# Performance work log

Measured on AMD Instinct MI355X. Metric: run time of the kernel, lower is better.

The kernel has to match this reference:

```python
import jax, jax.numpy as jnp
import numpy as np

N_NODES = 50000
N_EDGES = 800000
IN_CH = 64
OC = 16  # out_channels


def setup_inputs() -> dict:
    key = jax.random.key(0)
    ks = jax.random.split(key, 16)
    x = jax.random.normal(ks[0], (N_NODES, IN_CH), dtype=jnp.float32)
    edge_index = jax.random.randint(ks[1], (2, N_EDGES), 0, N_NODES, dtype=jnp.int64)

    def lin(k, fan_in, fan_out):
        s = 1.0 / np.sqrt(fan_in)
        return jax.random.uniform(k, (fan_in, fan_out), jnp.float32, -s, s)

    d1, d2 = 16 * OC, 8 * OC  # 256, 128
    return {
        "x": x,
        "W1_rel": lin(ks[2], IN_CH, d1), "b1": jnp.zeros((d1,), jnp.float32), "W1_root": lin(ks[3], IN_CH, d1),
        "W2_rel": lin(ks[4], d1, d2), "b2": jnp.zeros((d2,), jnp.float32), "W2_root": lin(ks[5], d1, d2),
        "Wmu_rel": lin(ks[6], d2, OC), "bmu": jnp.zeros((OC,), jnp.float32), "Wmu_root": lin(ks[7], d2, OC),
        "Wls_rel": lin(ks[8], d2, OC), "bls": jnp.zeros((OC,), jnp.float32), "Wls_root": lin(ks[9], d2, OC),
        "edge_index": edge_index,
    }


def _graph_conv(x, src, dst, deg_inv, W_rel, b, W_root):
    # PyG GraphConv(aggr='mean'): out = lin_rel(mean_{j in N(i)} x_j) + lin_root(x_i)
    msg_sum = jax.ops.segment_sum(x[src], dst, num_segments=x.shape[0])  # [N, d]
    agg = msg_sum * deg_inv[:, None]
    return agg @ W_rel + b + x @ W_root


def reference(x, W1_rel, b1, W1_root, W2_rel, b2, W2_root,
              Wmu_rel, bmu, Wmu_root, Wls_rel, bls, Wls_root, edge_index):
    src, dst = edge_index[0], edge_index[1]
    deg = jax.ops.segment_sum(jnp.ones_like(dst, dtype=x.dtype), dst, num_segments=x.shape[0])
    deg_inv = jnp.where(deg > 0, 1.0 / jnp.maximum(deg, 1.0), 0.0)

    h = jax.nn.relu(_graph_conv(x, src, dst, deg_inv, W1_rel, b1, W1_root))
    h = jax.nn.relu(_graph_conv(h, src, dst, deg_inv, W2_rel, b2, W2_root))
    mu = _graph_conv(h, src, dst, deg_inv, Wmu_rel, bmu, Wmu_root)
    logstd = _graph_conv(h, src, dst, deg_inv, Wls_rel, bls, Wls_root)
    return (mu, logstd)
```

## Files before the change

### kernel.cpp

```cpp
#include <hip/hip_runtime.h>
#include <hip/hip_fp8.h>

#define N_NODES 50000
#define N_EDGES 800000
#define NBUCK 196
#define PBLK 391
#define CAP 5120

typedef unsigned short ushort_t;
typedef unsigned char uchar_t;
typedef short short8 __attribute__((ext_vector_type(8)));
typedef short short4v __attribute__((ext_vector_type(4)));
typedef float floatx4 __attribute__((ext_vector_type(4)));
typedef float floatx2 __attribute__((ext_vector_type(2)));

__device__ __forceinline__ float bf2f(ushort_t u) {
    unsigned v = ((unsigned)u) << 16;
    return __builtin_bit_cast(float, v);
}
__device__ __forceinline__ ushort_t f2bf(float f) {
    unsigned u = __builtin_bit_cast(unsigned, f);
    unsigned r = (u + 0x7FFFu + ((u >> 16) & 1u)) >> 16;
    return (ushort_t)r;
}
__device__ __forceinline__ uchar_t f2fp8(float f) {
    return (uchar_t)(__builtin_amdgcn_cvt_pk_fp8_f32(f, f, 0, false) & 0xFF);
}
__device__ __forceinline__ float4 ld4(const float* p) { return *(const float4*)p; }

__device__ __forceinline__ void lite_barrier() {
    asm volatile("s_waitcnt lgkmcnt(0)" ::: "memory");
    __builtin_amdgcn_s_barrier();
}

__device__ __forceinline__ void acc16(float* a, uint4 v) {
    unsigned ws[4] = {v.x, v.y, v.z, v.w};
    #pragma unroll
    for (int wi = 0; wi < 4; ++wi) {
        floatx2 lo = __builtin_amdgcn_cvt_pk_f32_fp8(ws[wi], false);
        floatx2 hi = __builtin_amdgcn_cvt_pk_f32_fp8(ws[wi], true);
        a[wi * 4 + 0] += lo.x; a[wi * 4 + 1] += lo.y;
        a[wi * 4 + 2] += hi.x; a[wi * 4 + 3] += hi.y;
    }
}
__device__ __forceinline__ void acc8(float* a, uint2 v) {
    floatx2 p0 = __builtin_amdgcn_cvt_pk_f32_fp8(v.x, false);
    floatx2 p1 = __builtin_amdgcn_cvt_pk_f32_fp8(v.x, true);
    floatx2 p2 = __builtin_amdgcn_cvt_pk_f32_fp8(v.y, false);
    floatx2 p3 = __builtin_amdgcn_cvt_pk_f32_fp8(v.y, true);
    a[0] += p0.x; a[1] += p0.y; a[2] += p1.x; a[3] += p1.y;
    a[4] += p2.x; a[5] += p2.y; a[6] += p3.x; a[7] += p3.y;
}

__global__ __launch_bounds__(256) void prep_kernel(
    const float* __restrict__ x,
    const float* __restrict__ W1_rel, const float* __restrict__ W1_root,
    const float* __restrict__ W2_rel, const float* __restrict__ W2_root,
    const float* __restrict__ Wmu_rel, const float* __restrict__ Wls_rel,
    const float* __restrict__ Wmu_root, const float* __restrict__ Wls_root,
    ushort_t* __restrict__ xb, uchar_t* __restrict__ xq,
    ushort_t* __restrict__ B1t, ushort_t* __restrict__ B2t, ushort_t* __restrict__ B3t,
    int* __restrict__ bcursor) {
    int idx = blockIdx.x * blockDim.x + threadIdx.x;
    if (idx < 400000) {
        int n = idx >> 3, c = (idx & 7) * 8;
        float4 v0 = ld4(x + (size_t)n * 64 + c);
        float4 v1 = ld4(x + (size_t)n * 64 + c + 4);
        float vv[8] = {v0.x, v0.y, v0.z, v0.w, v1.x, v1.y, v1.z, v1.w};
        short8 o;
        #pragma unroll
        for (int i = 0; i < 8; ++i) o[i] = f2bf(vv[i]);
        int q0 = __builtin_amdgcn_cvt_pk_fp8_f32(vv[0], vv[1], 0, false);
        q0 = __builtin_amdgcn_cvt_pk_fp8_f32(vv[2], vv[3], q0, true);
        int q1 = __builtin_amdgcn_cvt_pk_fp8_f32(vv[4], vv[5], 0, false);
        q1 = __builtin_amdgcn_cvt_pk_fp8_f32(vv[6], vv[7], q1, true);
        *(short8*)(xb + (size_t)n * 64 + c) = o;
        uint2 q = {(unsigned)q0, (unsigned)q1};
        *(uint2*)(xq + (size_t)n * 64 + c) = q;
    } else if (idx < 506496) {
        int j = idx - 400000;
        if (j < 32768) {
            int n = j >> 7, k = j & 127;
            float v = (k < 64) ? W1_rel[k * 256 + n] : W1_root[(k - 64) * 256 + n];
            B1t[j] = f2bf(v);
        } else if (j < 98304) {
            int jj = j - 32768;
            int n = jj >> 8, k = jj & 255;
            float v = (n < 128) ? W2_rel[k * 128 + n] : W2_root[k * 128 + (n - 128)];
            B2t[jj] = f2bf(v);
        } else {
            int jj = j - 98304;
            int n = jj >> 7, k = jj & 127;
            const float* W = (n < 16) ? Wmu_rel : (n < 32) ? Wls_rel : (n < 48) ? Wmu_root : Wls_root;
            B3t[jj] = f2bf(W[k * 16 + (n & 15)]);
        }
    } else if (idx < 506496 + NBUCK) {
        int b = idx - 506496;
        bcursor[b] = b * CAP;
    }
}

__global__ __launch_bounds__(512) void partition_kernel(
    const int* __restrict__ src, const int* __restrict__ dst,
    int* __restrict__ bcursor, unsigned* __restrict__ pairbuf) {
    __shared__ int h[NBUCK];
    __shared__ int cur[NBUCK];
    const int tid = threadIdx.x;
    for (int i = tid; i < NBUCK; i += 512) h[i] = 0;
    __syncthreads();
    const int base = blockIdx.x * 2048;
    int d[4];
    #pragma unroll
    for (int j = 0; j < 4; ++j) {
        int e = base + j * 512 + tid;
        if (e < N_EDGES) { d[j] = dst[e]; atomicAdd(&h[d[j] >> 8], 1); }
        else d[j] = -1;
    }
    __syncthreads();
    for (int i = tid; i < NBUCK; i += 512) {
        int c = h[i];
        cur[i] = c ? atomicAdd(&bcursor[i], c) : 0;
    }
    __syncthreads();
    #pragma unroll
    for (int j = 0; j < 4; ++j) {
        int e = base + j * 512 + tid;
        if (e < N_EDGES) {
            int dd = d[j];
            int slot = atomicAdd(&cur[dd >> 8], 1);
            pairbuf[slot] = (unsigned)src[e] | ((unsigned)(dd & 255) << 16);
        }
    }
}

__global__ __launch_bounds__(1024) void fill_bucket_kernel(
    const unsigned* __restrict__ pairbuf, const int* __restrict__ bcursor,
    int* __restrict__ row_beg, int* __restrict__ row_end,
    float* __restrict__ dinv, ushort_t* __restrict__ eidx) {
    __shared__ int h[256];
    __shared__ int sm[256];
    __shared__ int cur[256];
    const int b = blockIdx.x, tid = threadIdx.x;
    const int beg = b * CAP, end = bcursor[b];
    if (tid < 256) h[tid] = 0;
    __syncthreads();
    for (int i = beg + tid; i < end; i += 1024)
        atomicAdd(&h[pairbuf[i] >> 16], 1);
    __syncthreads();
    if (tid < 256) sm[tid] = h[tid];
    __syncthreads();
    #pragma unroll
    for (int off = 1; off < 256; off <<= 1) {
        int t = 0;
        if (tid < 256 && tid >= off) t = sm[tid - off];
        __syncthreads();
        if (tid < 256) sm[tid] += t;
        __syncthreads();
    }
    if (tid < 256) {
        int c = h[tid];
        int exc = beg + sm[tid] - c;
        int node = b * 256 + tid;
        if (node < N_NODES) {
            row_beg[node] = exc;
            row_end[node] = exc + c;
            dinv[node] = c > 0 ? 1.0f / (float)c : 0.0f;
        }
        cur[tid] = exc;
    }
    __syncthreads();
    for (int i = beg + tid; i < end; i += 1024) {
        unsigned v = pairbuf[i];
        int slot = atomicAdd(&cur[v >> 16], 1);
        eidx[slot] = (ushort_t)(v & 0xFFFFu);
    }
}

__global__ __launch_bounds__(256, 3) void g1gemm12(
    const ushort_t* __restrict__ xb, const uchar_t* __restrict__ xq,
    const int* __restrict__ row_beg, const int* __restrict__ row_end,
    const ushort_t* __restrict__ eidx, const float* __restrict__ dinv,
    const ushort_t* __restrict__ B1t, const float* __restrict__ b1,
    const ushort_t* __restrict__ B2t,
    uchar_t* __restrict__ t2, ushort_t* __restrict__ r2) {
    constexpr int K1 = 128, K2 = 256;
    constexpr int AKP = 72;
    constexpr int HKP = 264;
    constexpr int BKP = 136;
    __shared__ ushort_t Bs[64 * BKP];
    __shared__ ushort_t Hs[64 * HKP];
    ushort_t* As = Bs;
    const int tid = threadIdx.x;
    const int rowbase = blockIdx.x * 64;

    {
        const int nl = tid >> 2, lane = tid & 3;
        const int node = rowbase + nl;
        int beg = 0, end = 0;
        float d = 0.0f;
        if (node < N_NODES) { beg = row_beg[node]; end = row_end[node]; d = dinv[node]; }
        float a0[16] = {}, a1[16] = {};
        int j = beg;
        for (; j + 3 < end; j += 4) {
            uint4 v0 = *(const uint4*)(xq + (size_t)eidx[j] * 64 + lane * 16);
            uint4 v1 = *(const uint4*)(xq + (size_t)eidx[j + 1] * 64 + lane * 16);
            uint4 v2 = *(const uint4*)(xq + (size_t)eidx[j + 2] * 64 + lane * 16);
            uint4 v3 = *(const uint4*)(xq + (size_t)eidx[j + 3] * 64 + lane * 16);
            acc16(a0, v0); acc16(a1, v1); acc16(a0, v2); acc16(a1, v3);
        }
        for (; j < end; ++j) {
            uint4 v0 = *(const uint4*)(xq + (size_t)eidx[j] * 64 + lane * 16);
            acc16(a0, v0);
        }
        short8 o0, o1;
        #pragma unroll
        for (int i = 0; i < 8; ++i) {
            o0[i] = f2bf((a0[i] + a1[i]) * d);
            o1[i] = f2bf((a0[8 + i] + a1[8 + i]) * d);
        }
        *(short8*)(As + nl * AKP + lane * 16) = o0;
        *(short8*)(As + nl * AKP + lane * 16 + 8) = o1;
    }
    __syncthreads();

    const int w = tid >> 6, lane64 = tid & 63;
    const int ln = lane64 & 15, quad = lane64 >> 4;
    const int rwl = w * 16 + ln;
    int r = rowbase + rwl;
    if (r > N_NODES - 1) r = N_NODES - 1;

    float bias[4][4];
    #pragma unroll
    for (int ny = 0; ny < 4; ++ny)
        #pragma unroll
        for (int f = 0; f < 4; ++f)
            bias[ny][f] = b1[ny * 64 + f * 16 + ln];

    short8 a[4];
    a[0] = *(const short8*)(As + rwl * AKP + quad * 8);
    a[1] = *(const short8*)(As + rwl * AKP + 32 + quad * 8);
    a[2] = *(const short8*)(xb + (size_t)r * 64 + quad * 8);
    a[3] = *(const short8*)(xb + (size_t)r * 64 + 32 + quad * 8);
    {
        short8 pb[4];
        #pragma unroll
        for (int i = 0; i < 4; ++i) {
            int idx = tid + i * 256, row = idx >> 4, off = (idx & 15) * 8;
            pb[i] = *(const short8*)(B1t + (size_t)row * K1 + off);
        }
        for (int ny = 0; ny < 4; ++ny) {
            lite_barrier();
            #pragma unroll
            for (int i = 0; i < 4; ++i) {
                int idx = tid + i * 256, row = idx >> 4, off = (idx & 15) * 8;
                *(short8*)(Bs + row * BKP + off) = pb[i];
            }
            if (ny < 3) {
                #pragma unroll
                for (int i = 0; i < 4; ++i) {
                    int idx = tid + i * 256, row = idx >> 4, off = (idx & 15) * 8;
                    pb[i] = *(const short8*)(B1t + (size_t)((ny + 1) * 64 + row) * K1 + off);
                }
            }
            lite_barrier();
            floatx4 acc[4] = {};
            #pragma unroll
            for (int f = 0; f < 4; ++f) {
                const ushort_t* bp = Bs + (f * 16 + ln) * BKP + quad * 8;
                #pragma unroll
                for (int s = 0; s < 4; ++s) {
                    short8 b = *(const short8*)(bp + s * 32);
                    acc[f] = __builtin_amdgcn_mfma_f32_16x16x32_bf16(a[s], b, acc[f], 0, 0, 0);
                }
            }
            #pragma unroll
            for (int f = 0; f < 4; ++f) {
                int n = ny * 64 + f * 16 + ln;
                #pragma unroll
                for (int g = 0; g < 4; ++g) {
                    int rr = w * 16 + quad * 4 + g;
                    Hs[rr * HKP + n] = f2bf(fmaxf(acc[f][g] + bias[ny][f], 0.0f));
                }
            }
        }
    }
    __syncthreads();

    short8 a2[8];
    #pragma unroll
    for (int s = 0; s < 8; ++s)
        a2[s] = *(const short8*)(Hs + rwl * HKP + s * 32 + quad * 8);
    ushort_t* Or16 = Hs;
    uchar_t*  Ot8  = (uchar_t*)(Hs + 8704);
    {
        short8 pb[4];
        #pragma unroll
        for (int i = 0; i < 4; ++i) {
            int idx = tid + i * 256, row = idx >> 4, off = (idx & 15) * 8;
            pb[i] = *(const short8*)(B2t + (size_t)row * K2 + off);
        }
        for (int ny = 0; ny < 4; ++ny) {
            floatx4 acc[4] = {};
            #pragma unroll
            for (int kh = 0; kh < 2; ++kh) {
                lite_barrier();
                #pragma unroll
                for (int i = 0; i < 4; ++i) {
                    int idx = tid + i * 256, row = idx >> 4, off = (idx & 15) * 8;
                    *(short8*)(Bs + row * BKP + off) = pb[i];
                }
                int st = ny * 2 + kh;
                if (st < 7) {
                    int nyn = (st + 1) >> 1, khn = (st + 1) & 1;
                    #pragma unroll
                    for (int i = 0; i < 4; ++i) {
                        int idx = tid + i * 256, row = idx >> 4, off = (idx & 15) * 8;
                        pb[i] = *(const short8*)(B2t + (size_t)(nyn * 64 + row) * K2 + khn * 128 + off);
                    }
                }
                lite_barrier();
                #pragma unroll
                for (int f = 0; f < 4; ++f) {
                    const ushort_t* bp = Bs + (f * 16 + ln) * BKP + quad * 8;
                    #pragma unroll
                    for (int s = 0; s < 4; ++s) {
                        short8 b = *(const short8*)(bp + s * 32);
                        acc[f] = __builtin_amdgcn_mfma_f32_16x16x32_bf16(a2[kh * 4 + s], b, acc[f], 0, 0, 0);
                    }
                }
            }
            #pragma unroll
            for (int f = 0; f < 4; ++f) {
                int n = ny * 64 + f * 16 + ln;
                #pragma unroll
                for (int g = 0; g < 4; ++g) {
                    int rr = w * 16 + quad * 4 + g;
                    float v = acc[f][g];
                    if (n < 128) Ot8[rr * 144 + n] = f2fp8(v);
                    else Or16[rr * 136 + (n - 128)] = f2bf(v);
                }
            }
        }
    }
    __syncthreads();

    {
        const int row = tid >> 2, seg = tid & 3;
        const int gr = rowbase + row;
        if (gr < N_NODES) {
            const uint4* ps = (const uint4*)(Ot8 + row * 144 + seg * 32);
            uint4* pd = (uint4*)(t2 + (size_t)gr * 128 + seg * 32);
            pd[0] = ps[0]; pd[1] = ps[1];
            const uint4* qs = (const uint4*)(Or16 + row * 136 + seg * 32);
            uint4* qd = (uint4*)(r2 + (size_t)gr * 128 + seg * 32);
            qd[0] = qs[0]; qd[1] = qs[1]; qd[2] = qs[2]; qd[3] = qs[3];
        }
    }
}

__global__ __launch_bounds__(256) void g2g3_kernel(
    const uchar_t* __restrict__ t2, const ushort_t* __restrict__ r2,
    const int* __restrict__ row_beg, const int* __restrict__ row_end,
    const ushort_t* __restrict__ eidx, const float* __restrict__ dinv,
    const float* __restrict__ b2, const ushort_t* __restrict__ B3t,
    ushort_t* __restrict__ tml, float* __restrict__ rml) {
    constexpr int KP = 136;
    __shared__ ushort_t As[16 * KP];
    const int tid = threadIdx.x;
    const int nb = blockIdx.x * 16;
    {
        const int nl = tid >> 4, lane = tid & 15;
        const int node = nb + nl;
        const int beg = row_beg[node], end = row_end[node];
        float a0[8] = {}, a1[8] = {}, a2[8] = {}, a3[8] = {};
        int j = beg;
        for (; j + 3 < end; j += 4) {
            uint2 v0 = *(const uint2*)(t2 + (size_t)eidx[j] * 128 + lane * 8);
            uint2 v1 = *(const uint2*)(t2 + (size_t)eidx[j + 1] * 128 + lane * 8);
            uint2 v2 = *(const uint2*)(t2 + (size_t)eidx[j + 2] * 128 + lane * 8);
            uint2 v3 = *(const uint2*)(t2 + (size_t)eidx[j + 3] * 128 + lane * 8);
            acc8(a0, v0); acc8(a1, v1); acc8(a2, v2); acc8(a3, v3);
        }
        for (; j < end; ++j) {
            uint2 v0 = *(const uint2*)(t2 + (size_t)eidx[j] * 128 + lane * 8);
            acc8(a0, v0);
        }
        float d = dinv[node];
        short8 rv = *(const short8*)(r2 + (size_t)node * 128 + lane * 8);
        float4 ba = ld4(b2 + lane * 8), bb = ld4(b2 + lane * 8 + 4);
        float bc[8] = {ba.x, ba.y, ba.z, ba.w, bb.x, bb.y, bb.z, bb.w};
        short8 o;
        #pragma unroll
        for (int i = 0; i < 8; ++i)
            o[i] = f2bf(fmaxf(((a0[i] + a1[i]) + (a2[i] + a3[i])) * d + bf2f((ushort_t)rv[i]) + bc[i], 0.0f));
        *(short8*)(As + nl * KP + lane * 8) = o;
    }
    __syncthreads();
    const int w = tid >> 6, lane64 = tid & 63;
    const int ln = lane64 & 15, quad = lane64 >> 4;
    short8 a[4];
    #pragma unroll
    for (int s = 0; s < 4; ++s)
        a[s] = *(const short8*)(As + ln * KP + s * 32 + quad * 8);
    floatx4 acc = {};
    const ushort_t* bp = B3t + (size_t)(w * 16 + ln) * 128 + quad * 8;
    #pragma unroll
    for (int s = 0; s < 4; ++s) {
        short8 b = *(const short8*)(bp + s * 32);
        acc = __builtin_amdgcn_mfma_f32_16x16x32_bf16(a[s], b, acc, 0, 0, 0);
    }
    const int r0 = nb + quad * 4;
    const int ncol = w * 16 + ln;
    #pragma unroll
    for (int g = 0; g < 4; ++g) {
        int rr = r0 + g;
        float v = acc[g];
        if (ncol < 32) tml[(size_t)rr * 32 + ncol] = f2bf(v);
        else rml[(size_t)rr * 32 + (ncol - 32)] = v;
    }
}

__global__ __launch_bounds__(256) void gather3_kernel(
    const ushort_t* __restrict__ tml, const float* __restrict__ rml,
    const int* __restrict__ row_beg, const int* __restrict__ row_end,
    const ushort_t* __restrict__ eidx, const float* __restrict__ dinv,
    const float* __restrict__ bmu, const float* __restrict__ bls,
    float* __restrict__ out) {
    const int lane = threadIdx.x & 7;
    const int nl = threadIdx.x >> 3;
    const int n = blockIdx.x * 32 + nl;
    if (n >= N_NODES) return;
    const int beg = row_beg[n], end = row_end[n];
    float a0[4] = {}, a1[4] = {}, a2[4] = {}, a3[4] = {};
    int j = beg;
    for (; j + 3 < end; j += 4) {
        short4v v0 = *(const short4v*)(tml + (size_t)eidx[j] * 32 + lane * 4);
        short4v v1 = *(const short4v*)(tml + (size_t)eidx[j + 1] * 32 + lane * 4);
        short4v v2 = *(const short4v*)(tml + (size_t)eidx[j + 2] * 32 + lane * 4);
        short4v v3 = *(const short4v*)(tml + (size_t)eidx[j + 3] * 32 + lane * 4);
        #pragma unroll
        for (int i = 0; i < 4; ++i) {
            a0[i] += bf2f((ushort_t)v0[i]); a1[i] += bf2f((ushort_t)v1[i]);
            a2[i] += bf2f((ushort_t)v2[i]); a3[i] += bf2f((ushort_t)v3[i]);
        }
    }
    for (; j < end; ++j) {
        short4v v0 = *(const short4v*)(tml + (size_t)eidx[j] * 32 + lane * 4);
        #pragma unroll
        for (int i = 0; i < 4; ++i) a0[i] += bf2f((ushort_t)v0[i]);
    }
    float d = dinv[n];
    const float* bias = (lane < 4) ? (bmu + lane * 4) : (bls + (lane - 4) * 4);
    float4 ra = ld4(rml + (size_t)n * 32 + lane * 4);
    float4 ba = ld4(bias);
    float rr[4] = {ra.x, ra.y, ra.z, ra.w};
    float bc[4] = {ba.x, ba.y, ba.z, ba.w};
    float res[4];
    #pragma unroll
    for (int i = 0; i < 4; ++i) res[i] = ((a0[i] + a1[i]) + (a2[i] + a3[i])) * d + rr[i] + bc[i];
    float* base = (lane < 4) ? (out + (size_t)n * 16 + lane * 4)
                             : (out + 800000u + (size_t)n * 16 + (lane - 4) * 4);
    *(float4*)(base) = make_float4(res[0], res[1], res[2], res[3]);
}

extern "C" void kernel_launch(void* const* d_in, const int* in_sizes, int n_in,
                              void* d_out, int out_size, void* d_ws, size_t ws_size,
                              hipStream_t stream) {
    const float* x       = (const float*)d_in[0];
    const float* W1_rel  = (const float*)d_in[1];
    const float* b1      = (const float*)d_in[2];
    const float* W1_root = (const float*)d_in[3];
    const float* W2_rel  = (const float*)d_in[4];
    const float* b2      = (const float*)d_in[5];
    const float* W2_root = (const float*)d_in[6];
    const float* Wmu_rel = (const float*)d_in[7];
    const float* bmu     = (const float*)d_in[8];
    const float* Wmu_root= (const float*)d_in[9];
    const float* Wls_rel = (const float*)d_in[10];
    const float* bls     = (const float*)d_in[11];
    const float* Wls_root= (const float*)d_in[12];
    const int*   ei      = (const int*)d_in[13];
    const int* src = ei;
    const int* dst = ei + N_EDGES;

    int*      bcursor = (int*)d_ws;
    int*      row_beg = bcursor + 256;
    int*      row_end = row_beg + 50048;
    unsigned* pairbuf = (unsigned*)(row_end + 50048);
    ushort_t* eidx    = (ushort_t*)(pairbuf + 1003520);
    float*    dinv    = (float*)(eidx + 1003520);
    ushort_t* xb   = (ushort_t*)(dinv + 50000);
    uchar_t*  xq   = (uchar_t*)(xb + 3200000);
    uchar_t*  t2   = xq + 3200000;
    ushort_t* r2   = (ushort_t*)(t2 + 6400000);
    ushort_t* tml  = r2 + 6400000;
    ushort_t* B1t  = tml + 1600000;
    ushort_t* B2t  = B1t + 32768;
    ushort_t* B3t  = B2t + 65536;
    float* rml     = (float*)(B3t + 8192);
    float* out     = (float*)d_out;

    prep_kernel<<<1980, 256, 0, stream>>>(x, W1_rel, W1_root, W2_rel, W2_root,
                                          Wmu_rel, Wls_rel, Wmu_root, Wls_root,
                                          xb, xq, B1t, B2t, B3t, bcursor);
    partition_kernel<<<PBLK, 512, 0, stream>>>(src, dst, bcursor, pairbuf);
    fill_bucket_kernel<<<NBUCK, 1024, 0, stream>>>(pairbuf, bcursor, row_beg, row_end, dinv, eidx);

    g1gemm12<<<782, 256, 0, stream>>>(xb, xq, row_beg, row_end, eidx, dinv,
                                      B1t, b1, B2t, t2, r2);

    g2g3_kernel<<<3125, 256, 0, stream>>>(t2, r2, row_beg, row_end, eidx, dinv, b2, B3t, tml, rml);

    gather3_kernel<<<1563, 256, 0, stream>>>(tml, rml, row_beg, row_end, eidx, dinv, bmu, bls, out);
}
```

Measured before the change: 194.6 us.

## Spill layer-1 hidden tile to global scratch to shrink shared memory footprint

Removes the 64x264 bf16 shared buffer for the layer-1 hidden activations and writes each 64-column chunk to a global scratch buffer h1g through the small Bs staging area. The second GEMM then loads its A operand straight from global memory. The aim is to cut LDS per block, from roughly 51KB to roughly 17KB, so more blocks fit per CU. The cost is extra global write and read traffic, since the reads should mostly hit in L2, plus more barriers. The launch-bounds occupancy hint is also dropped.

Result: no change. 192.7 us (-1.0%).

```diff
diff --git a/kernel.cpp b/kernel.cpp
--- a/kernel.cpp
+++ b/kernel.cpp
@@ -176,19 +176,17 @@
     }
 }
 
-__global__ __launch_bounds__(256, 3) void g1gemm12(
+__global__ __launch_bounds__(256) void g1gemm12(
     const ushort_t* __restrict__ xb, const uchar_t* __restrict__ xq,
     const int* __restrict__ row_beg, const int* __restrict__ row_end,
     const ushort_t* __restrict__ eidx, const float* __restrict__ dinv,
     const ushort_t* __restrict__ B1t, const float* __restrict__ b1,
-    const ushort_t* __restrict__ B2t,
+    const ushort_t* __restrict__ B2t, ushort_t* __restrict__ h1g,
     uchar_t* __restrict__ t2, ushort_t* __restrict__ r2) {
     constexpr int K1 = 128, K2 = 256;
     constexpr int AKP = 72;
-    constexpr int HKP = 264;
     constexpr int BKP = 136;
     __shared__ ushort_t Bs[64 * BKP];
-    __shared__ ushort_t Hs[64 * HKP];
     ushort_t* As = Bs;
     const int tid = threadIdx.x;
     const int rowbase = blockIdx.x * 64;
@@ -241,119 +239,136 @@
     a[1] = *(const short8*)(As + rwl * AKP + 32 + quad * 8);
     a[2] = *(const short8*)(xb + (size_t)r * 64 + quad * 8);
     a[3] = *(const short8*)(xb + (size_t)r * 64 + 32 + quad * 8);
-    {
-        short8 pb[4];
+    short8 pb[4];
+    #pragma unroll
+    for (int i = 0; i < 4; ++i) {
+        int idx = tid + i * 256, row = idx >> 4, off = (idx & 15) * 8;
+        pb[i] = *(const short8*)(B1t + (size_t)row * K1 + off);
+    }
+    for (int ny = 0; ny < 4; ++ny) {
+        lite_barrier();
         #pragma unroll
         for (int i = 0; i < 4; ++i) {
             int idx = tid + i * 256, row = idx >> 4, off = (idx & 15) * 8;
-            pb[i] = *(const short8*)(B1t + (size_t)row * K1 + off);
-        }
-        for (int ny = 0; ny < 4; ++ny) {
+            *(short8*)(Bs + row * BKP + off) = pb[i];
+        }
+        if (ny < 3) {
+            #pragma unroll
+            for (int i = 0; i < 4; ++i) {
+                int idx = tid + i * 256, row = idx >> 4, off = (idx & 15) * 8;
+                pb[i] = *(const short8*)(B1t + (size_t)((ny + 1) * 64 + row) * K1 + off);
+            }
+        } else {
+            #pragma unroll
+            for (int i = 0; i < 4; ++i) {
+                int idx = tid + i * 256, row = idx >> 4, off = (idx & 15) * 8;
+                pb[i] = *(const short8*)(B2t + (size_t)row * K2 + off);
+            }
+        }
+        lite_barrier();
+        floatx4 acc[4] = {};
+        #pragma unroll
+        for (int f = 0; f < 4; ++f) {
+            const ushort_t* bp = Bs + (f * 16 + ln) * BKP + quad * 8;
+            #pragma unroll
+            for (int s = 0; s < 4; ++s) {
+                short8 b = *(const short8*)(bp + s * 32);
+                acc[f] = __builtin_amdgcn_mfma_f32_16x16x32_bf16(a[s], b, acc[f], 0, 0, 0);
+            }
+        }
+        lite_barrier();
+        #pragma unroll
+        for (int f = 0; f < 4; ++f) {
+            int nl0 = f * 16 + ln;
+            #pragma unroll
+            for (int g = 0; g < 4; ++g) {
+                int rr = w * 16 + quad * 4 + g;
+                Bs[rr * AKP + nl0] = f2bf(fmaxf(acc[f][g] + bias[ny][f], 0.0f));
+            }
+        }
+        lite_barrier();
+        {
+            int row2 = tid >> 2, seg = tid & 3;
+            int gr = rowbase + row2;
+            if (gr < N_NODES) {
+                const uint4* s4 = (const uint4*)(Bs + row2 * AKP + seg * 16);
+                uint4* d4 = (uint4*)(h1g + (size_t)gr * 256 + ny * 64 + seg * 16);
+                d4[0] = s4[0]; d4[1] = s4[1];
+            }
+        }
+    }
+    __syncthreads();
+
+    short8 a2[8];
+    #pragma unroll
+    for (int s = 0; s < 8; ++s)
+        a2[s] = *(const short8*)(h1g + (size_t)r * 256 + s * 32 + quad * 8);
+    for (int ny = 0; ny < 4; ++ny) {
+        floatx4 acc[4] = {};
+        #pragma unroll
+        for (int kh = 0; kh < 2; ++kh) {
             lite_barrier();
             #pragma unroll
             for (int i = 0; i < 4; ++i) {
                 int idx = tid + i * 256, row = idx >> 4, off = (idx & 15) * 8;
                 *(short8*)(Bs + row * BKP + off) = pb[i];
             }
-            if (ny < 3) {
+            int st = ny * 2 + kh;
+            if (st < 7) {
+                int nyn = (st + 1) >> 1, khn = (st + 1) & 1;
                 #pragma unroll
                 for (int i = 0; i < 4; ++i) {
                     int idx = tid + i * 256, row = idx >> 4, off = (idx & 15) * 8;
-                    pb[i] = *(const short8*)(B1t + (size_t)((ny + 1) * 64 + row) * K1 + off);
+                    pb[i] = *(const short8*)(B2t + (size_t)(nyn * 64 + row) * K2 + khn * 128 + off);
                 }
             }
             lite_barrier();
-            floatx4 acc[4] = {};
             #pragma unroll
             for (int f = 0; f < 4; ++f) {
                 const ushort_t* bp = Bs + (f * 16 + ln) * BKP + quad * 8;
                 #pragma unroll
                 for (int s = 0; s < 4; ++s) {
                     short8 b = *(const short8*)(bp + s * 32);
-                    acc[f] = __builtin_amdgcn_mfma_f32_16x16x32_bf16(a[s], b, acc[f], 0, 0, 0);
+                    acc[f] = __builtin_amdgcn_mfma_f32_16x16x32_bf16(a2[kh * 4 + s], b, acc[f], 0, 0, 0);
                 }
             }
+        }
+        lite_barrier();
+        if (ny < 2) {
+            uchar_t* Ob = (uchar_t*)Bs;
             #pragma unroll
             for (int f = 0; f < 4; ++f) {
-                int n = ny * 64 + f * 16 + ln;
+                int nl0 = f * 16 + ln;
                 #pragma unroll
                 for (int g = 0; g < 4; ++g) {
                     int rr = w * 16 + quad * 4 + g;
-                    Hs[rr * HKP + n] = f2bf(fmaxf(acc[f][g] + bias[ny][f], 0.0f));
+                    Ob[rr * 80 + nl0] = f2fp8(acc[f][g]);
                 }
             }
-        }
-    }
-    __syncthreads();
-
-    short8 a2[8];
-    #pragma unroll
-    for (int s = 0; s < 8; ++s)
-        a2[s] = *(const short8*)(Hs + rwl * HKP + s * 32 + quad * 8);
-    ushort_t* Or16 = Hs;
-    uchar_t*  Ot8  = (uchar_t*)(Hs + 8704);
-    {
-        short8 pb[4];
-        #pragma unroll
-        for (int i = 0; i < 4; ++i) {
-            int idx = tid + i * 256, row = idx >> 4, off = (idx & 15) * 8;
-            pb[i] = *(const short8*)(B2t + (size_t)row * K2 + off);
-        }
-        for (int ny = 0; ny < 4; ++ny) {
-            floatx4 acc[4] = {};
-            #pragma unroll
-            for (int kh = 0; kh < 2; ++kh) {
-                lite_barrier();
-                #pragma unroll
-                for (int i = 0; i < 4; ++i) {
-                    int idx = tid + i * 256, row = idx >> 4, off = (idx & 15) * 8;
-                    *(short8*)(Bs + row * BKP + off) = pb[i];
-                }
-                int st = ny * 2 + kh;
-                if (st < 7) {
-                    int nyn = (st + 1) >> 1, khn = (st + 1) & 1;
-                    #pragma unroll
-                    for (int i = 0; i < 4; ++i) {
-                        int idx = tid + i * 256, row = idx >> 4, off = (idx & 15) * 8;
-                        pb[i] = *(const short8*)(B2t + (size_t)(nyn * 64 + row) * K2 + khn * 128 + off);
-                    }
-                }
-                lite_barrier();
-                #pragma unroll
-                for (int f = 0; f < 4; ++f) {
-                    const ushort_t* bp = Bs + (f * 16 + ln) * BKP + quad * 8;
-                    #pragma unroll
-                    for (int s = 0; s < 4; ++s) {
-                        short8 b = *(const short8*)(bp + s * 32);
-                        acc[f] = __builtin_amdgcn_mfma_f32_16x16x32_bf16(a2[kh * 4 + s], b, acc[f], 0, 0, 0);
-                    }
-                }
-            }
+            lite_barrier();
+            int row2 = tid >> 2, seg = tid & 3;
+            int gr = rowbase + row2;
+            if (gr < N_NODES)
+                *(uint4*)(t2 + (size_t)gr * 128 + ny * 64 + seg * 16) =
+                    *(const uint4*)(Ob + row2 * 80 + seg * 16);
+        } else {
             #pragma unroll
             for (int f = 0; f < 4; ++f) {
-                int n = ny * 64 + f * 16 + ln;
+                int nl0 = f * 16 + ln;
                 #pragma unroll
                 for (int g = 0; g < 4; ++g) {
                     int rr = w * 16 + quad * 4 + g;
-                    float v = acc[f][g];
-                    if (n < 128) Ot8[rr * 144 + n] = f2fp8(v);
-                    else Or16[rr * 136 + (n - 128)] = f2bf(v);
+                    Bs[rr * AKP + nl0] = f2bf(acc[f][g]);
                 }
             }
-        }
-    }
-    __syncthreads();
-
-    {
-        const int row = tid >> 2, seg = tid & 3;
-        const int gr = rowbase + row;
-        if (gr < N_NODES) {
-            const uint4* ps = (const uint4*)(Ot8 + row * 144 + seg * 32);
-            uint4* pd = (uint4*)(t2 + (size_t)gr * 128 + seg * 32);
-            pd[0] = ps[0]; pd[1] = ps[1];
-            const uint4* qs = (const uint4*)(Or16 + row * 136 + seg * 32);
-            uint4* qd = (uint4*)(r2 + (size_t)gr * 128 + seg * 32);
-            qd[0] = qs[0]; qd[1] = qs[1]; qd[2] = qs[2]; qd[3] = qs[3];
+            lite_barrier();
+            int row2 = tid >> 2, seg = tid & 3;
+            int gr = rowbase + row2;
+            if (gr < N_NODES) {
+                const uint4* s4 = (const uint4*)(Bs + row2 * AKP + seg * 16);
+                uint4* d4 = (uint4*)(r2 + (size_t)gr * 128 + (ny - 2) * 64 + seg * 16);
+                d4[0] = s4[0]; d4[1] = s4[1];
+            }
         }
     }
 }
@@ -498,6 +513,7 @@
     ushort_t* B2t  = B1t + 32768;
     ushort_t* B3t  = B2t + 65536;
     float* rml     = (float*)(B3t + 8192);
+    ushort_t* h1g  = (ushort_t*)(rml + 1600000);
     float* out     = (float*)d_out;
 
     prep_kernel<<<1980, 256, 0, stream>>>(x, W1_rel, W1_root, W2_rel, W2_root,
@@ -507,7 +523,7 @@
     fill_bucket_kernel<<<NBUCK, 1024, 0, stream>>>(pairbuf, bcursor, row_beg, row_end, dinv, eidx);
 
     g1gemm12<<<782, 256, 0, stream>>>(xb, xq, row_beg, row_end, eidx, dinv,
-                                      B1t, b1, B2t, t2, r2);
+                                      B1t, b1, B2t, h1g, t2, r2);
 
     g2g3_kernel<<<3125, 256, 0, stream>>>(t2, r2, row_beg, row_end, eidx, dinv, b2, B3t, tml, rml);
 
```
